# Performance work log

Measured on AMD Instinct MI355X. Metric: run time of the kernel, lower is better.

The kernel has to match this reference:

```python
import jax, jax.numpy as jnp
import numpy as np

N_NODES = 50000
N_EDGES = 1600000
IN_DIM = 128
HEADS = 4
HID = 16
NEG_SLOPE = 0.2  # DGL GATConv default


def setup_inputs() -> dict:
    key = jax.random.key(0)
    ks = jax.random.split(key, 7)
    features = jax.random.normal(ks[0], (N_NODES, IN_DIM), dtype=jnp.float32)
    W = jax.random.normal(ks[1], (IN_DIM, HEADS * HID), dtype=jnp.float32) * 0.1
    attn_l = jax.random.normal(ks[2], (HEADS, HID), dtype=jnp.float32) * 0.1
    attn_r = jax.random.normal(ks[3], (HEADS, HID), dtype=jnp.float32) * 0.1
    bias = jax.random.normal(ks[4], (HEADS * HID,), dtype=jnp.float32) * 0.1
    src = jax.random.randint(ks[5], (N_EDGES,), 0, N_NODES, dtype=jnp.int64)
    dst = jax.random.randint(ks[6], (N_EDGES,), 0, N_NODES, dtype=jnp.int64)
    return {"features": features, "W": W, "attn_l": attn_l, "attn_r": attn_r,
            "bias": bias, "src": src, "dst": dst}


def reference(features, W, attn_l, attn_r, bias, src, dst):
    N = features.shape[0]
    H, D = attn_l.shape
    # linear projection -> per-head features [N, H, D]
    feat = (features @ W).reshape(N, H, D)
    el = jnp.einsum('nhd,hd->nh', feat, attn_l)  # [N, H]
    er = jnp.einsum('nhd,hd->nh', feat, attn_r)  # [N, H]
    # per-edge unnormalized attention logits [E, H]
    e = jax.nn.leaky_relu(el[src] + er[dst], negative_slope=NEG_SLOPE)
    # edge softmax segmented by destination node (numerically stable)
    emax = jax.ops.segment_max(e, dst, num_segments=N)
    ee = jnp.exp(e - emax[dst])
    denom = jax.ops.segment_sum(ee, dst, num_segments=N)
    alpha = ee / denom[dst]  # [E, H]
    # weighted neighbor aggregation: scatter-add of alpha * feat[src]
    msg = feat[src] * alpha[:, :, None]  # [E, H, D]
    out = jax.ops.segment_sum(msg, dst, num_segments=N)  # [N, H, D]
    out = out + bias.reshape(1, H, D)
    # wrapper GAT.forward averages over heads
    return out.mean(axis=1)  # [N, D]
```

## Files before the change

### kernel.cpp

```cpp
#include <hip/hip_runtime.h>
#include <hip/hip_bf16.h>

#define IN_DIM 128
#define HEADS 4
#define HID 16
#define HD 64
#define NEG_SLOPE 0.2f
#define PSHIFT 7
#define PCAP 5120
#define NPMAX 512
#define EPB 4096
#define NB_PROJ 768

typedef __attribute__((ext_vector_type(8))) short bf16x8;
typedef __attribute__((ext_vector_type(4))) float f32x4;

__device__ __forceinline__ float lrelu_exp(float x) {
    float e = x > 0.0f ? x : NEG_SLOPE * x;
    return __expf(e);
}

__device__ __forceinline__ unsigned short f2bf(float x) {
    unsigned int u = __float_as_uint(x);
    return (unsigned short)((u + 0x7fffu + ((u >> 16) & 1u)) >> 16);
}

__global__ __launch_bounds__(256) void k_prjpart(const float* __restrict__ features,
                                                 const float* __restrict__ W,
                                                 const float* __restrict__ attn_l,
                                                 const float* __restrict__ attn_r,
                                                 __hip_bfloat16* __restrict__ feat16,
                                                 float* __restrict__ el,
                                                 float* __restrict__ er,
                                                 const int* __restrict__ src,
                                                 const int* __restrict__ dst,
                                                 int* __restrict__ cursor,
                                                 unsigned int* __restrict__ partbuf,
                                                 int n_nodes, int n_edges,
                                                 int npart, int npartblk) {
    __shared__ float smem[IN_DIM * HD];

    if (blockIdx.x < (unsigned)npartblk) {
        int* hist = (int*)smem;
        int* base = (int*)smem + NPMAX;
        const int t = threadIdx.x;
        for (int i = t; i < npart; i += 256) hist[i] = 0;
        __syncthreads();

        const int e0 = blockIdx.x * EPB;
        unsigned int vals[16];
#pragma unroll
        for (int j = 0; j < 4; ++j) {
            int e = e0 + j * 1024 + t * 4;
            if (e + 4 <= n_edges) {
                int4 s4 = *reinterpret_cast<const int4*>(src + e);
                int4 d4 = *reinterpret_cast<const int4*>(dst + e);
                vals[j * 4 + 0] = ((unsigned)d4.x << 16) | (unsigned)s4.x;
                vals[j * 4 + 1] = ((unsigned)d4.y << 16) | (unsigned)s4.y;
                vals[j * 4 + 2] = ((unsigned)d4.z << 16) | (unsigned)s4.z;
                vals[j * 4 + 3] = ((unsigned)d4.w << 16) | (unsigned)s4.w;
            } else {
#pragma unroll
                for (int k = 0; k < 4; ++k) {
                    int ee = e + k;
                    vals[j * 4 + k] = (ee < n_edges)
                        ? (((unsigned)dst[ee] << 16) | (unsigned)src[ee])
                        : 0xffffffffu;
                }
            }
        }
#pragma unroll
        for (int j = 0; j < 16; ++j)
            if (vals[j] != 0xffffffffu) atomicAdd(&hist[vals[j] >> (16 + PSHIFT)], 1);
        __syncthreads();
        for (int i = t; i < npart; i += 256) {
            base[i] = atomicAdd(&cursor[i], hist[i]);
            hist[i] = 0;
        }
        __syncthreads();
#pragma unroll
        for (int j = 0; j < 16; ++j) {
            unsigned int v = vals[j];
            if (v != 0xffffffffu) {
                int p = v >> (16 + PSHIFT);
                int idx = base[p] + atomicAdd(&hist[p], 1);
                if (idx < PCAP) partbuf[(size_t)p * PCAP + idx] = v;
            }
        }
        return;
    }

    float* Wl = smem;
    for (int i = threadIdx.x; i < IN_DIM * HD; i += 256) Wl[i] = W[i];
    __syncthreads();

    const int lane  = threadIdx.x & 63;
    const int wave  = threadIdx.x >> 6;
    const int colid = lane & 15;
    const int quad  = lane >> 4;

    float al[4], ar[4];
#pragma unroll
    for (int c = 0; c < 4; ++c) {
        al[c] = attn_l[c * 16 + colid];
        ar[c] = attn_r[c * 16 + colid];
    }

    bf16x8 bf[16];
#pragma unroll
    for (int c = 0; c < 4; ++c) {
#pragma unroll
        for (int q = 0; q < 4; ++q) {
            bf16x8 v;
#pragma unroll
            for (int j = 0; j < 8; ++j) {
                int k = q * 32 + quad * 8 + j;
                v[j] = (short)f2bf(Wl[k * HD + c * 16 + colid]);
            }
            bf[c * 4 + q] = v;
        }
    }

    const int ngroups = (n_nodes + 15) >> 4;
    const int gwave = (blockIdx.x - npartblk) * 4 + wave;
    const int nwaves = NB_PROJ * 4;

    for (int g = gwave; g < ngroups; g += nwaves) {
        const int n0 = g * 16;
        int rown = n0 + colid;
        if (rown >= n_nodes) rown = n_nodes - 1;
        const float* fp = features + (size_t)rown * IN_DIM + quad * 8;

        f32x4 acc0 = {0.f, 0.f, 0.f, 0.f};
        f32x4 acc1 = {0.f, 0.f, 0.f, 0.f};
        f32x4 acc2 = {0.f, 0.f, 0.f, 0.f};
        f32x4 acc3 = {0.f, 0.f, 0.f, 0.f};
#pragma unroll
        for (int q = 0; q < 4; ++q) {
            float4 a0 = *reinterpret_cast<const float4*>(fp + q * 32);
            float4 a1 = *reinterpret_cast<const float4*>(fp + q * 32 + 4);
            bf16x8 av;
            av[0] = (short)f2bf(a0.x); av[1] = (short)f2bf(a0.y);
            av[2] = (short)f2bf(a0.z); av[3] = (short)f2bf(a0.w);
            av[4] = (short)f2bf(a1.x); av[5] = (short)f2bf(a1.y);
            av[6] = (short)f2bf(a1.z); av[7] = (short)f2bf(a1.w);
            acc0 = __builtin_amdgcn_mfma_f32_16x16x32_bf16(av, bf[0 * 4 + q], acc0, 0, 0, 0);
            acc1 = __builtin_amdgcn_mfma_f32_16x16x32_bf16(av, bf[1 * 4 + q], acc1, 0, 0, 0);
            acc2 = __builtin_amdgcn_mfma_f32_16x16x32_bf16(av, bf[2 * 4 + q], acc2, 0, 0, 0);
            acc3 = __builtin_amdgcn_mfma_f32_16x16x32_bf16(av, bf[3 * 4 + q], acc3, 0, 0, 0);
        }

        f32x4 accs[4] = {acc0, acc1, acc2, acc3};
        const bool full = (n0 + 16 <= n_nodes);
#pragma unroll
        for (int c = 0; c < 4; ++c) {
            f32x4 v = accs[c];
#pragma unroll
            for (int r = 0; r < 4; ++r) {
                int n = n0 + quad * 4 + r;
                if (full || n < n_nodes) {
                    ((unsigned short*)feat16)[(size_t)n * HD + c * 16 + colid] = f2bf(v[r]);
                }
            }
            float pl0 = v[0] * al[c], pl1 = v[1] * al[c], pl2 = v[2] * al[c], pl3 = v[3] * al[c];
            float pr0 = v[0] * ar[c], pr1 = v[1] * ar[c], pr2 = v[2] * ar[c], pr3 = v[3] * ar[c];
#pragma unroll
            for (int m = 1; m < 16; m <<= 1) {
                pl0 += __shfl_xor(pl0, m); pl1 += __shfl_xor(pl1, m);
                pl2 += __shfl_xor(pl2, m); pl3 += __shfl_xor(pl3, m);
                pr0 += __shfl_xor(pr0, m); pr1 += __shfl_xor(pr1, m);
                pr2 += __shfl_xor(pr2, m); pr3 += __shfl_xor(pr3, m);
            }
            if (colid == 0) {
                int nb = n0 + quad * 4;
                if (full) {
                    el[(size_t)(nb + 0) * HEADS + c] = pl0;
                    el[(size_t)(nb + 1) * HEADS + c] = pl1;
                    el[(size_t)(nb + 2) * HEADS + c] = pl2;
                    el[(size_t)(nb + 3) * HEADS + c] = pl3;
                    er[(size_t)(nb + 0) * HEADS + c] = pr0;
                    er[(size_t)(nb + 1) * HEADS + c] = pr1;
                    er[(size_t)(nb + 2) * HEADS + c] = pr2;
                    er[(size_t)(nb + 3) * HEADS + c] = pr3;
                } else {
                    float pls[4] = {pl0, pl1, pl2, pl3};
                    float prs[4] = {pr0, pr1, pr2, pr3};
                    for (int r = 0; r < 4; ++r) {
                        if (nb + r < n_nodes) {
                            el[(size_t)(nb + r) * HEADS + c] = pls[r];
                            er[(size_t)(nb + r) * HEADS + c] = prs[r];
                        }
                    }
                }
            }
        }
    }
}

__global__ __launch_bounds__(512) void k_sort(const unsigned int* __restrict__ partbuf,
                                              const int* __restrict__ cursor,
                                              unsigned short* __restrict__ csr,
                                              int* __restrict__ row_ptr,
                                              unsigned short* __restrict__ deg16,
                                              int n_nodes) {
    __shared__ int hist[128];
    __shared__ int scan_s[128];
    const int p = blockIdx.x;
    const int t = threadIdx.x;
    const int count = min(cursor[p], PCAP);
    const unsigned int* buf = partbuf + (size_t)p * PCAP;

    unsigned int vals[10];
#pragma unroll
    for (int j = 0; j < 10; ++j) {
        int i = t + j * 512;
        vals[j] = (i < count) ? buf[i] : 0xffffffffu;
    }

    if (t < 128) hist[t] = 0;
    __syncthreads();
#pragma unroll
    for (int j = 0; j < 10; ++j)
        if (vals[j] != 0xffffffffu) atomicAdd(&hist[(vals[j] >> 16) & 127], 1);
    __syncthreads();

    int v = 0;
    if (t < 128) {
        v = hist[t];
        scan_s[t] = v;
    }
    __syncthreads();
    for (int off = 1; off < 128; off <<= 1) {
        int u = (t >= off && t < 128) ? scan_s[t - off] : 0;
        __syncthreads();
        if (t < 128) scan_s[t] += u;
        __syncthreads();
    }
    if (t < 128) {
        const int excl = scan_s[t] - v;
        const int node = (p << PSHIFT) + t;
        if (node < n_nodes) {
            row_ptr[node] = p * PCAP + excl;
            deg16[node] = (unsigned short)v;
        }
        hist[t] = excl;
    }
    __syncthreads();
    unsigned short* cbase = csr + (size_t)p * PCAP;
#pragma unroll
    for (int j = 0; j < 10; ++j) {
        unsigned int val = vals[j];
        if (val != 0xffffffffu) {
            int ld = (val >> 16) & 127;
            int pos = atomicAdd(&hist[ld], 1);
            cbase[pos] = (unsigned short)(val & 0xffffu);
        }
    }
}

__global__ __launch_bounds__(256) void k_agg(const int* __restrict__ row_ptr,
                                             const unsigned short* __restrict__ deg16,
                                             const unsigned short* __restrict__ csr,
                                             const float* __restrict__ el,
                                             const float* __restrict__ er,
                                             const unsigned int* __restrict__ feat16u,
                                             const float* __restrict__ bias,
                                             float* __restrict__ out,
                                             int n_nodes) {
    int n = (blockIdx.x * blockDim.x + threadIdx.x) >> 6;
    if (n >= n_nodes) return;
    const int lane = threadIdx.x & 63;
    const int half = lane >> 5;
    const int sub = lane & 31;
    const int h = sub >> 3;
    const int eW = lane >> 2;
    const int hW = lane & 3;

    const int beg = row_ptr[n];
    const int deg = (int)deg16[n];
    const unsigned short* row = csr + beg;
    const float erW = er[(size_t)n * HEADS + hW];

    const int baseLane = half * 4 + h;

    float nx0 = 0.f, ny0 = 0.f, nx1 = 0.f, ny1 = 0.f;
    float denacc = 0.f;

    bool valid = (eW < deg);
    int s = valid ? (int)row[eW] : 0;
    float w = valid ? lrelu_exp(el[(size_t)s * HEADS + hW] + erW) : 0.f;

    for (int i0 = 0; i0 < deg; i0 += 16) {
        denacc += w;
        const unsigned int pw = ((unsigned int)f2bf(w) << 16) | (unsigned int)s;

        unsigned int pk[8];
#pragma unroll
        for (int j = 0; j < 8; ++j) pk[j] = __shfl(pw, baseLane + (j << 3));

        const bool v2 = (i0 + 16 + eW < deg);
        int s2 = v2 ? (int)row[i0 + 16 + eW] : 0;

        unsigned int pf[8];
#pragma unroll
        for (int j = 0; j < 8; ++j)
            pf[j] = feat16u[((pk[j] & 0xffffu) << 5) + sub];

        float w2 = v2 ? lrelu_exp(el[(size_t)s2 * HEADS + hW] + erW) : 0.f;

#pragma unroll
        for (int j = 0; j < 8; ++j) {
            float wj = __uint_as_float(pk[j] & 0xffff0000u);
            if (j & 1) {
                nx1 = fmaf(wj, __uint_as_float(pf[j] << 16), nx1);
                ny1 = fmaf(wj, __uint_as_float(pf[j] & 0xffff0000u), ny1);
            } else {
                nx0 = fmaf(wj, __uint_as_float(pf[j] << 16), nx0);
                ny0 = fmaf(wj, __uint_as_float(pf[j] & 0xffff0000u), ny0);
            }
        }
        s = s2;
        w = w2;
    }

    float den = denacc;
    den += __shfl_xor(den, 4);
    den += __shfl_xor(den, 8);
    den += __shfl_xor(den, 16);
    den += __shfl_xor(den, 32);
    float denh = __shfl(den, h);

    float nx = nx0 + nx1, ny = ny0 + ny1;
    nx += __shfl_xor(nx, 32);
    ny += __shfl_xor(ny, 32);
    float inv = (denh > 0.f) ? 0.25f / denh : 0.f;
    float rx = nx * inv;
    float ry = ny * inv;
    rx += __shfl_xor(rx, 8);
    ry += __shfl_xor(ry, 8);
    rx += __shfl_xor(rx, 16);
    ry += __shfl_xor(ry, 16);
    if (lane < 8) {
        int dp = lane;
        float bx = 0.25f * (bias[2 * dp] + bias[HID + 2 * dp] +
                            bias[2 * HID + 2 * dp] + bias[3 * HID + 2 * dp]);
        float by = 0.25f * (bias[2 * dp + 1] + bias[HID + 2 * dp + 1] +
                            bias[2 * HID + 2 * dp + 1] + bias[3 * HID + 2 * dp + 1]);
        *reinterpret_cast<float2*>(out + (size_t)n * HID + 2 * dp) =
            make_float2(rx + bx, ry + by);
    }
}

extern "C" void kernel_launch(void* const* d_in, const int* in_sizes, int n_in,
                              void* d_out, int out_size, void* d_ws, size_t ws_size,
                              hipStream_t stream) {
    const float* features = (const float*)d_in[0];
    const float* W        = (const float*)d_in[1];
    const float* attn_l   = (const float*)d_in[2];
    const float* attn_r   = (const float*)d_in[3];
    const float* bias     = (const float*)d_in[4];
    const int*   src      = (const int*)d_in[5];
    const int*   dst      = (const int*)d_in[6];
    float* out = (float*)d_out;

    const int n_nodes = in_sizes[0] / IN_DIM;
    const int n_edges = in_sizes[5];
    const int npart = (n_nodes + (1 << PSHIFT) - 1) >> PSHIFT;
    const int npartblk = (n_edges + EPB - 1) / EPB;

    char* ws = (char*)d_ws;
    __hip_bfloat16* feat16 = (__hip_bfloat16*)ws; ws += (size_t)n_nodes * HD * sizeof(__hip_bfloat16);
    float* el      = (float*)ws;                  ws += (size_t)n_nodes * HEADS * sizeof(float);
    float* er      = (float*)ws;                  ws += (size_t)n_nodes * HEADS * sizeof(float);
    unsigned int* partbuf = (unsigned int*)ws;    ws += (size_t)npart * PCAP * sizeof(unsigned int);
    unsigned short* csr = (unsigned short*)ws;    ws += (size_t)npart * PCAP * sizeof(unsigned short);
    int* row_ptr   = (int*)ws;                    ws += (size_t)n_nodes * sizeof(int);
    unsigned short* deg16 = (unsigned short*)ws;  ws += (size_t)n_nodes * sizeof(unsigned short);
    int* cursor    = (int*)ws;                    ws += NPMAX * sizeof(int);

    hipMemsetAsync(cursor, 0, NPMAX * sizeof(int), stream);

    k_prjpart<<<npartblk + NB_PROJ, 256, 0, stream>>>(features, W, attn_l, attn_r,
                                                      feat16, el, er, src, dst,
                                                      cursor, partbuf,
                                                      n_nodes, n_edges, npart, npartblk);
    k_sort<<<npart, 512, 0, stream>>>(partbuf, cursor, csr, row_ptr, deg16, n_nodes);
    k_agg<<<(n_nodes + 3) / 4, 256, 0, stream>>>(row_ptr, deg16, csr, el, er,
                                                 (const unsigned int*)feat16, bias, out, n_nodes);
}
```

Baseline: 163.8 us.

## Fold attention projections into a fifth MFMA tile and stage weight fragments in LDS

Precomputes W·attn_l and W·attn_r as extra bf16 columns so el/er come out of a fifth MFMA tile instead of per-head shuffle reductions. Weight fragments are prebuilt once per block into shared memory and read per group, instead of being held in 16 registers per lane. This removes the xor-shuffle reduction chains and lowers register pressure, at the cost of one extra MFMA and LDS reads per group. el/er now come from bf16-rounded folded weights, which changes numerics slightly.

```diff
diff --git a/kernel.cpp b/kernel.cpp
--- a/kernel.cpp
+++ b/kernel.cpp
@@ -11,6 +11,7 @@
 #define NPMAX 512
 #define EPB 4096
 #define NB_PROJ 768
+#define NTILE 5
 
 typedef __attribute__((ext_vector_type(8))) short bf16x8;
 typedef __attribute__((ext_vector_type(4))) float f32x4;
@@ -90,36 +91,63 @@
         return;
     }
 
-    float* Wl = smem;
-    for (int i = threadIdx.x; i < IN_DIM * HD; i += 256) Wl[i] = W[i];
-    __syncthreads();
-
+    for (int i = threadIdx.x; i < IN_DIM * HD; i += 256) smem[i] = W[i];
+    __syncthreads();
+
+    uint4 ent[NTILE];
+#pragma unroll
+    for (int i = 0; i < NTILE; ++i) {
+        const int e  = threadIdx.x + (i << 8);
+        const int fi = e >> 6;
+        const int ln = e & 63;
+        const int c  = fi >> 2;
+        const int q  = fi & 3;
+        const int colid = ln & 15;
+        const int quad  = ln >> 4;
+        unsigned short v[8];
+        if (c < 4) {
+#pragma unroll
+            for (int j = 0; j < 8; ++j) {
+                int k = q * 32 + quad * 8 + j;
+                v[j] = f2bf(smem[k * HD + c * 16 + colid]);
+            }
+        } else if (colid < 8) {
+            const int h = colid & 3;
+            const float* attn = (colid < 4) ? attn_l : attn_r;
+            float at[16];
+#pragma unroll
+            for (int d = 0; d < 16; ++d) at[d] = attn[h * 16 + d];
+#pragma unroll
+            for (int j = 0; j < 8; ++j) {
+                int k = q * 32 + quad * 8 + j;
+                float sum = 0.f;
+#pragma unroll
+                for (int d = 0; d < 16; ++d)
+                    sum = fmaf(smem[k * HD + h * 16 + d], at[d], sum);
+                v[j] = f2bf(sum);
+            }
+        } else {
+#pragma unroll
+            for (int j = 0; j < 8; ++j) v[j] = 0;
+        }
+        ent[i].x = (unsigned int)v[0] | ((unsigned int)v[1] << 16);
+        ent[i].y = (unsigned int)v[2] | ((unsigned int)v[3] << 16);
+        ent[i].z = (unsigned int)v[4] | ((unsigned int)v[5] << 16);
+        ent[i].w = (unsigned int)v[6] | ((unsigned int)v[7] << 16);
+    }
+    __syncthreads();
+
+    uint4* fragw = (uint4*)smem;
+#pragma unroll
+    for (int i = 0; i < NTILE; ++i)
+        fragw[threadIdx.x + (i << 8)] = ent[i];
+    __syncthreads();
+
+    const bf16x8* frags = (const bf16x8*)smem;
     const int lane  = threadIdx.x & 63;
     const int wave  = threadIdx.x >> 6;
     const int colid = lane & 15;
     const int quad  = lane >> 4;
-
-    float al[4], ar[4];
-#pragma unroll
-    for (int c = 0; c < 4; ++c) {
-        al[c] = attn_l[c * 16 + colid];
-        ar[c] = attn_r[c * 16 + colid];
-    }
-
-    bf16x8 bf[16];
-#pragma unroll
-    for (int c = 0; c < 4; ++c) {
-#pragma unroll
-        for (int q = 0; q < 4; ++q) {
-            bf16x8 v;
-#pragma unroll
-            for (int j = 0; j < 8; ++j) {
-                int k = q * 32 + quad * 8 + j;
-                v[j] = (short)f2bf(Wl[k * HD + c * 16 + colid]);
-            }
-            bf[c * 4 + q] = v;
-        }
-    }
 
     const int ngroups = (n_nodes + 15) >> 4;
     const int gwave = (blockIdx.x - npartblk) * 4 + wave;
@@ -131,10 +159,10 @@
         if (rown >= n_nodes) rown = n_nodes - 1;
         const float* fp = features + (size_t)rown * IN_DIM + quad * 8;
 
-        f32x4 acc0 = {0.f, 0.f, 0.f, 0.f};
-        f32x4 acc1 = {0.f, 0.f, 0.f, 0.f};
-        f32x4 acc2 = {0.f, 0.f, 0.f, 0.f};
-        f32x4 acc3 = {0.f, 0.f, 0.f, 0.f};
+        f32x4 acc[NTILE];
+#pragma unroll
+        for (int c = 0; c < NTILE; ++c) acc[c] = (f32x4){0.f, 0.f, 0.f, 0.f};
+
 #pragma unroll
         for (int q = 0; q < 4; ++q) {
             float4 a0 = *reinterpret_cast<const float4*>(fp + q * 32);
@@ -144,53 +172,32 @@
             av[2] = (short)f2bf(a0.z); av[3] = (short)f2bf(a0.w);
             av[4] = (short)f2bf(a1.x); av[5] = (short)f2bf(a1.y);
             av[6] = (short)f2bf(a1.z); av[7] = (short)f2bf(a1.w);
-            acc0 = __builtin_amdgcn_mfma_f32_16x16x32_bf16(av, bf[0 * 4 + q], acc0, 0, 0, 0);
-            acc1 = __builtin_amdgcn_mfma_f32_16x16x32_bf16(av, bf[1 * 4 + q], acc1, 0, 0, 0);
-            acc2 = __builtin_amdgcn_mfma_f32_16x16x32_bf16(av, bf[2 * 4 + q], acc2, 0, 0, 0);
-            acc3 = __builtin_amdgcn_mfma_f32_16x16x32_bf16(av, bf[3 * 4 + q], acc3, 0, 0, 0);
-        }
-
-        f32x4 accs[4] = {acc0, acc1, acc2, acc3};
+#pragma unroll
+            for (int c = 0; c < NTILE; ++c) {
+                bf16x8 bv = frags[(c * 4 + q) * 64 + lane];
+                acc[c] = __builtin_amdgcn_mfma_f32_16x16x32_bf16(av, bv, acc[c], 0, 0, 0);
+            }
+        }
+
         const bool full = (n0 + 16 <= n_nodes);
 #pragma unroll
         for (int c = 0; c < 4; ++c) {
-            f32x4 v = accs[c];
 #pragma unroll
             for (int r = 0; r < 4; ++r) {
                 int n = n0 + quad * 4 + r;
                 if (full || n < n_nodes) {
-                    ((unsigned short*)feat16)[(size_t)n * HD + c * 16 + colid] = f2bf(v[r]);
+                    ((unsigned short*)feat16)[(size_t)n * HD + c * 16 + colid] = f2bf(acc[c][r]);
                 }
             }
-            float pl0 = v[0] * al[c], pl1 = v[1] * al[c], pl2 = v[2] * al[c], pl3 = v[3] * al[c];
-            float pr0 = v[0] * ar[c], pr1 = v[1] * ar[c], pr2 = v[2] * ar[c], pr3 = v[3] * ar[c];
-#pragma unroll
-            for (int m = 1; m < 16; m <<= 1) {
-                pl0 += __shfl_xor(pl0, m); pl1 += __shfl_xor(pl1, m);
-                pl2 += __shfl_xor(pl2, m); pl3 += __shfl_xor(pl3, m);
-                pr0 += __shfl_xor(pr0, m); pr1 += __shfl_xor(pr1, m);
-                pr2 += __shfl_xor(pr2, m); pr3 += __shfl_xor(pr3, m);
-            }
-            if (colid == 0) {
-                int nb = n0 + quad * 4;
-                if (full) {
-                    el[(size_t)(nb + 0) * HEADS + c] = pl0;
-                    el[(size_t)(nb + 1) * HEADS + c] = pl1;
-                    el[(size_t)(nb + 2) * HEADS + c] = pl2;
-                    el[(size_t)(nb + 3) * HEADS + c] = pl3;
-                    er[(size_t)(nb + 0) * HEADS + c] = pr0;
-                    er[(size_t)(nb + 1) * HEADS + c] = pr1;
-                    er[(size_t)(nb + 2) * HEADS + c] = pr2;
-                    er[(size_t)(nb + 3) * HEADS + c] = pr3;
-                } else {
-                    float pls[4] = {pl0, pl1, pl2, pl3};
-                    float prs[4] = {pr0, pr1, pr2, pr3};
-                    for (int r = 0; r < 4; ++r) {
-                        if (nb + r < n_nodes) {
-                            el[(size_t)(nb + r) * HEADS + c] = pls[r];
-                            er[(size_t)(nb + r) * HEADS + c] = prs[r];
-                        }
-                    }
+        }
+        if (colid < 8) {
+            float* dstp = (colid < 4) ? el : er;
+            const int h = colid & 3;
+#pragma unroll
+            for (int r = 0; r < 4; ++r) {
+                int n = n0 + quad * 4 + r;
+                if (full || n < n_nodes) {
+                    dstp[(size_t)n * HEADS + h] = acc[4][r];
                 }
             }
         }
```

Result: faster. 159.9 us (-2.4%).
